# Kernel optimization log

Hardware: AMD Instinct MI355X
Metric: run time of the kernel (lower is better)

## Reference

```python
import jax, jax.numpy as jnp
import numpy as np

BLOCK_SIZE = 32
HEADS = 8
DIM_HEAD = 64
ROPE_THETA = 10000.0


def rmsnorm(x, w):
    eps = jnp.finfo(x.dtype).eps
    var = jnp.mean(jnp.square(x), axis=-1, keepdims=True)
    return x * jax.lax.rsqrt(var + eps) * w


def rope_cos_sin(seq_len, dim_head):
    # lucidrains rotary-embedding-torch default: interleaved pairs, theta=10000
    inv_freq = 1.0 / (ROPE_THETA ** (jnp.arange(0, dim_head, 2, dtype=jnp.float32) / dim_head))
    freqs = jnp.arange(seq_len, dtype=jnp.float32)[:, None] * inv_freq[None, :]  # [S, Dh/2]
    return jnp.cos(freqs), jnp.sin(freqs)


def apply_rope(t, cos, sin):
    # t: [B, H, S, Dh], cos/sin: [S, Dh/2]
    t1 = t[..., 0::2]
    t2 = t[..., 1::2]
    out = jnp.stack([t1 * cos - t2 * sin, t1 * sin + t2 * cos], axis=-1)
    return out.reshape(t.shape)


def split_heads(x, h):
    b, n, _ = x.shape
    return x.reshape(b, n, h, -1).transpose(0, 2, 1, 3)  # b h n d


def forward(tokens, attn_norm_w, qkv_w, out_w, mix_w, mix_b,
            ff_norm_w, ff_in_w, ff_in_b, ff_out_w, ff_out_b, final_norm_w):
    B, S, D = tokens.shape
    L = qkv_w.shape[0]
    H, Dh = HEADS, DIM_HEAD
    scale = Dh ** -0.5
    cos, sin = rope_cos_sin(S, Dh)

    # block-causal mask: q_idx // block >= kv_idx // block
    idx = jnp.arange(S)
    allowed = (idx[:, None] // BLOCK_SIZE) >= (idx[None, :] // BLOCK_SIZE)  # [S, S] bool
    neg = -jnp.finfo(tokens.dtype).max

    t = tokens
    first_v = None
    for l in range(L):
        # --- block causal attention ---
        x = rmsnorm(t, attn_norm_w[l])
        qkv = x @ qkv_w[l]  # [B, S, 3*H*Dh]
        q, k, v = jnp.split(qkv, 3, axis=-1)
        q, k, v = split_heads(q, H), split_heads(k, H), split_heads(v, H)  # b h s d
        orig_v = v
        if l > 0:
            mix = jax.nn.sigmoid(x @ mix_w[l] + mix_b[l])  # [B, S, H]
            mix = mix.transpose(0, 2, 1)[..., None]  # [B, H, S, 1]
            v = v + mix * (first_v - v)  # lerp
        q = apply_rope(q, cos, sin)
        k = apply_rope(k, cos, sin)
        sim = jnp.einsum('bhid,bhjd->bhij', q * scale, k)
        sim = jnp.where(allowed, sim, neg)
        attn = jax.nn.softmax(sim, axis=-1)
        o = jnp.einsum('bhij,bhjd->bhid', attn, v)
        o = o.transpose(0, 2, 1, 3).reshape(B, S, H * Dh)
        t = t + o @ out_w[l]
        if first_v is None:
            first_v = orig_v
        # --- SwiGLU feedforward ---
        y = rmsnorm(t, ff_norm_w[l])
        h = y @ ff_in_w[l] + ff_in_b[l]
        a, g = jnp.split(h, 2, axis=-1)
        y = (a * jax.nn.gelu(g, approximate=False)) @ ff_out_w[l] + ff_out_b[l]
        t = t + y

    return rmsnorm(t, final_norm_w)


def setup_inputs():
    key = jax.random.key(0)
    B, S, D, L = 2, 2048, 512, 4
    Di = HEADS * DIM_HEAD  # 512
    Dhid = int(D * 4.0 * 2 / 3)  # 1365
    ks = jax.random.split(key, 8)
    s = 0.02
    return {
        'tokens': jax.random.normal(ks[0], (B, S, D), jnp.float32),
        'attn_norm_w': jnp.ones((L, D), jnp.float32),
        'qkv_w': jax.random.normal(ks[1], (L, D, 3 * Di), jnp.float32) * s,
        'out_w': jax.random.normal(ks[2], (L, Di, D), jnp.float32) * s,
        'mix_w': jax.random.normal(ks[3], (L, D, HEADS), jnp.float32) * s,
        'mix_b': jnp.zeros((L, HEADS), jnp.float32),
        'ff_norm_w': jnp.ones((L, D), jnp.float32),
        'ff_in_w': jax.random.normal(ks[4], (L, D, 2 * Dhid), jnp.float32) * s,
        'ff_in_b': jnp.zeros((L, 2 * Dhid), jnp.float32),
        'ff_out_w': jax.random.normal(ks[5], (L, Dhid, D), jnp.float32) * s,
        'ff_out_b': jnp.zeros((L, D), jnp.float32),
        'final_norm_w': jnp.ones((D,), jnp.float32),
    }


def reference(tokens, attn_norm_w, qkv_w, out_w, mix_w, mix_b,
              ff_norm_w, ff_in_w, ff_in_b, ff_out_w, ff_out_b, final_norm_w):
    return forward(tokens, attn_norm_w, qkv_w, out_w, mix_w, mix_b,
                   ff_norm_w, ff_in_w, ff_in_b, ff_out_w, ff_out_b, final_norm_w)
```

## Files before the change

kernel.cpp:

```cpp
#include <hip/hip_runtime.h>
#include <hip/hip_bf16.h>
#include <math.h>

typedef __bf16 bf16;
typedef bf16 bf16x8 __attribute__((ext_vector_type(8)));
typedef float f32x4 __attribute__((ext_vector_type(4)));

#define LDS16(gp, lp) __builtin_amdgcn_global_load_lds( \
    (const __attribute__((address_space(1))) unsigned int*)(gp), \
    (__attribute__((address_space(3))) unsigned int*)(lp), 16, 0, 0)

__device__ __forceinline__ int cumoff2(int qtp) {
  if (qtp < 4)  return qtp;
  if (qtp < 8)  return 4 + 2 * (qtp - 4);
  if (qtp < 12) return 12 + 3 * (qtp - 8);
  return 24 + 4 * (qtp - 12);
}

__global__ void convert_w_kernel(const float* __restrict__ W, bf16* __restrict__ WT,
                                 int K, int N, int Kp, int Np,
                                 size_t wstride, size_t wtstride)
{
  __shared__ float tile[32][33];
  const float* Wl = W + blockIdx.z * wstride;
  bf16* WTl = WT + blockIdx.z * wtstride;
  int k0 = blockIdx.x * 32, n0 = blockIdx.y * 32;
  int tx = threadIdx.x, ty = threadIdx.y;
  for (int i = ty; i < 32; i += 8) {
    int k = k0 + i, n = n0 + tx;
    tile[i][tx] = (k < K && n < N) ? Wl[(size_t)k * N + n] : 0.f;
  }
  __syncthreads();
  for (int i = ty; i < 32; i += 8) {
    int n = n0 + i, k = k0 + tx;
    if (n < Np && k < Kp) WTl[(size_t)n * Kp + k] = (bf16)tile[tx][i];
  }
}

__global__ void convert_w_ffin_kernel(const float* __restrict__ W, bf16* __restrict__ WT)
{
  __shared__ float tile[32][33];
  const float* Wl = W + (size_t)blockIdx.z * 512 * 2730;
  bf16* WTl = WT + (size_t)blockIdx.z * 2816 * 512;
  int k0 = blockIdx.x * 32, n0 = blockIdx.y * 32;
  int tx = threadIdx.x, ty = threadIdx.y;
  for (int i = ty; i < 32; i += 8) {
    int k = k0 + i, n = n0 + tx;
    int pair = n >> 1;
    int col = (n & 1) ? 1365 + pair : pair;
    tile[i][tx] = (pair < 1365) ? Wl[(size_t)k * 2730 + col] : 0.f;
  }
  __syncthreads();
  for (int i = ty; i < 32; i += 8) {
    int n = n0 + i, k = k0 + tx;
    WTl[(size_t)n * 512 + k] = (bf16)tile[tx][i];
  }
}

__global__ __launch_bounds__(256)
void ibias_kernel(const float* __restrict__ ffib, float* __restrict__ ib)
{
  int idx = blockIdx.x * 256 + threadIdx.x;
  int l = idx / 2816, n = idx - l * 2816;
  int pair = n >> 1;
  int col = (n & 1) ? 1365 + pair : pair;
  ib[idx] = (pair < 1365) ? ffib[l * 2730 + col] : 0.f;
}

__global__ __launch_bounds__(256)
void rope_kernel(float* __restrict__ tab)
{
  int idx = blockIdx.x * 256 + threadIdx.x;
  int s = idx >> 5, j = idx & 31;
  float invf = (float)exp((double)(2 * j) * -0.14391156847064293);
  float ang = (float)s * invf;
  float sn, cs;
  sincosf(ang, &sn, &cs);
  tab[idx] = cs;
  tab[65536 + idx] = sn;
}

template<bool BF16OUT>
__global__ __launch_bounds__(256)
void rmsnorm_kernel(const float* __restrict__ in, const float* __restrict__ wgt,
                    void* __restrict__ outp)
{
  int row = blockIdx.x * 4 + (threadIdx.x >> 6);
  int lane = threadIdx.x & 63;
  const float* p = in + (size_t)row * 512;
  float4 v0 = *(const float4*)(p + lane * 4);
  float4 v1 = *(const float4*)(p + 256 + lane * 4);
  float ss = v0.x*v0.x + v0.y*v0.y + v0.z*v0.z + v0.w*v0.w
           + v1.x*v1.x + v1.y*v1.y + v1.z*v1.z + v1.w*v1.w;
  #pragma unroll
  for (int d = 1; d < 64; d <<= 1) ss += __shfl_xor(ss, d);
  float sc = rsqrtf(ss * (1.f / 512.f) + 1.1920929e-7f);
  float a0[4] = {v0.x, v0.y, v0.z, v0.w};
  float a1[4] = {v1.x, v1.y, v1.z, v1.w};
  #pragma unroll
  for (int i = 0; i < 4; ++i) {
    int c0 = lane * 4 + i, c1 = 256 + lane * 4 + i;
    float r0 = a0[i] * sc * wgt[c0];
    float r1 = a1[i] * sc * wgt[c1];
    if (BF16OUT) {
      ((bf16*)outp)[(size_t)row * 512 + c0] = (bf16)r0;
      ((bf16*)outp)[(size_t)row * 512 + c1] = (bf16)r1;
    } else {
      ((float*)outp)[(size_t)row * 512 + c0] = r0;
      ((float*)outp)[(size_t)row * 512 + c1] = r1;
    }
  }
}

__global__ __launch_bounds__(256, 4)
void qkvpost_kernel(const bf16* __restrict__ qkv, const float* __restrict__ mb,
                    const float* __restrict__ rope, bf16* __restrict__ firstv,
                    bf16* __restrict__ qb, bf16* __restrict__ kb,
                    bf16* __restrict__ vT, int layer)
{
  __shared__ float smv[64][65];
  const int st = blockIdx.x, bh = blockIdx.y;
  const int b = bh >> 3, h = bh & 7;
  const int tid = threadIdx.x;
  const int sl = tid >> 2, dg = tid & 3;
  const int s = st * 64 + sl;
  const size_t row = (size_t)b * 2048 + s;
  const bf16* base = qkv + row * 1664 + h * 64 + dg * 16;

  bf16x8 qv0 = *(const bf16x8*)(base);
  bf16x8 qv1 = *(const bf16x8*)(base + 8);
  bf16x8 kv0 = *(const bf16x8*)(base + 512);
  bf16x8 kv1 = *(const bf16x8*)(base + 520);
  bf16x8 vv0 = *(const bf16x8*)(base + 1024);
  bf16x8 vv1 = *(const bf16x8*)(base + 1032);

  float cs8[8], sn8[8];
  #pragma unroll
  for (int j = 0; j < 8; ++j) {
    cs8[j] = rope[s * 32 + dg * 8 + j];
    sn8[j] = rope[65536 + s * 32 + dg * 8 + j];
  }

  const size_t qoff = ((size_t)bh * 2048 + s) * 64 + dg * 16;
  bf16x8 oq0, oq1, ok0, ok1;
  #pragma unroll
  for (int p = 0; p < 4; ++p) {
    float q1 = (float)qv0[2 * p], q2 = (float)qv0[2 * p + 1];
    float k1 = (float)kv0[2 * p], k2 = (float)kv0[2 * p + 1];
    oq0[2 * p]     = (bf16)((q1 * cs8[p] - q2 * sn8[p]) * 0.125f);
    oq0[2 * p + 1] = (bf16)((q1 * sn8[p] + q2 * cs8[p]) * 0.125f);
    ok0[2 * p]     = (bf16)(k1 * cs8[p] - k2 * sn8[p]);
    ok0[2 * p + 1] = (bf16)(k1 * sn8[p] + k2 * cs8[p]);
    float q3 = (float)qv1[2 * p], q4v = (float)qv1[2 * p + 1];
    float k3 = (float)kv1[2 * p], k4 = (float)kv1[2 * p + 1];
    oq1[2 * p]     = (bf16)((q3 * cs8[p + 4] - q4v * sn8[p + 4]) * 0.125f);
    oq1[2 * p + 1] = (bf16)((q3 * sn8[p + 4] + q4v * cs8[p + 4]) * 0.125f);
    ok1[2 * p]     = (bf16)(k3 * cs8[p + 4] - k4 * sn8[p + 4]);
    ok1[2 * p + 1] = (bf16)(k3 * sn8[p + 4] + k4 * cs8[p + 4]);
  }
  *(bf16x8*)(qb + qoff)     = oq0;
  *(bf16x8*)(qb + qoff + 8) = oq1;
  *(bf16x8*)(kb + qoff)     = ok0;
  *(bf16x8*)(kb + qoff + 8) = ok1;

  float vout[16];
  #pragma unroll
  for (int i = 0; i < 8; ++i) { vout[i] = (float)vv0[i]; vout[8 + i] = (float)vv1[i]; }
  if (layer == 0) {
    *(bf16x8*)(firstv + qoff)     = vv0;
    *(bf16x8*)(firstv + qoff + 8) = vv1;
  } else {
    float logit = (float)qkv[row * 1664 + 1536 + h] + mb[h];
    float mx = 1.f / (1.f + __expf(-logit));
    bf16x8 fv0 = *(const bf16x8*)(firstv + qoff);
    bf16x8 fv1 = *(const bf16x8*)(firstv + qoff + 8);
    #pragma unroll
    for (int i = 0; i < 8; ++i) {
      vout[i]     += mx * ((float)fv0[i] - vout[i]);
      vout[8 + i] += mx * ((float)fv1[i] - vout[8 + i]);
    }
  }
  #pragma unroll
  for (int i = 0; i < 16; ++i)
    smv[sl][dg * 16 + i] = vout[i];

  __syncthreads();

  const int d = tid >> 2, q4 = tid & 3;
  bf16x8 o0, o1;
  #pragma unroll
  for (int i = 0; i < 8; ++i) {
    o0[i] = (bf16)smv[q4 * 16 + i][d];
    o1[i] = (bf16)smv[q4 * 16 + 8 + i][d];
  }
  bf16* vp = vT + ((size_t)bh * 64 + d) * 2048 + st * 64 + q4 * 16;
  *(bf16x8*)(vp)     = o0;
  *(bf16x8*)(vp + 8) = o1;
}

__global__ __launch_bounds__(256, 2)
void attn_kernel(const bf16* __restrict__ Q, const bf16* __restrict__ Kmat,
                 const bf16* __restrict__ VT, bf16* __restrict__ Opart,
                 float* __restrict__ lbuf)
{
  __shared__ __align__(16) bf16 smK[3][8 * 512];
  __shared__ __align__(16) bf16 smV[3][8 * 512];
  __shared__ __align__(16) bf16 smP[4][2][16 * 72];
  const int bid = blockIdx.x;
  const int bh = bid & 15;
  const int cidx = bid >> 4;
  int qtp, chunk;
  if (cidx < 4)       { qtp = cidx; chunk = 0; }
  else if (cidx < 12) { qtp = 4 + ((cidx - 4) >> 1);  chunk = (cidx - 4) & 1; }
  else if (cidx < 24) { int t = cidx - 12; qtp = 8 + t / 3; chunk = t - (qtp - 8) * 3; }
  else                { int t = cidx - 24; qtp = 12 + (t >> 2); chunk = t & 3; }
  const int jt0 = chunk * 8;
  const int njt = min(jt0 + 8, 2 * qtp + 2) - jt0;

  const int tid = threadIdx.x;
  const int w = tid >> 6, lane = tid & 63;
  const int c = lane & 15, quad = lane >> 4;
  const int jtmax_w = (qtp * 4 + w) >> 1;

  const size_t qrow0 = (size_t)bh * 2048 + qtp * 128 + w * 32;
  bf16x8 aQ[2][2];
  #pragma unroll
  for (int m = 0; m < 2; ++m) {
    aQ[m][0] = *(const bf16x8*)(Q + (qrow0 + m * 16 + c) * 64 + quad * 8);
    aQ[m][1] = *(const bf16x8*)(Q + (qrow0 + m * 16 + c) * 64 + 32 + quad * 8);
  }

  const bf16* Kg = Kmat + ((size_t)bh * 2048 + w * 16 + c) * 64 + quad * 8;
  const bf16* Vg = VT + ((size_t)bh * 64 + w * 16 + c) * 2048 + quad * 8;

  auto stage = [&](int tile, int buf) {
    const bf16* kp = Kg + (size_t)tile * 4096;
    const bf16* vp = Vg + tile * 64;
    bf16* kd = smK[buf] + w * 1024;
    bf16* vd = smV[buf] + w * 1024;
    LDS16(kp,      kd);
    LDS16(kp + 32, kd + 512);
    LDS16(vp,      vd);
    LDS16(vp + 32, vd + 512);
  };
  stage(jt0, 0);
  if (njt > 1) stage(jt0 + 1, 1);

  f32x4 o[2][4] = {};
  float lacc[2][4] = {};

  for (int j = 0; j < njt; ++j) {
    const int bufc = j % 3;
    const int jt = jt0 + j;
    if (j + 1 < njt) asm volatile("s_waitcnt vmcnt(4)\n\ts_barrier" ::: "memory");
    else             asm volatile("s_waitcnt vmcnt(0)\n\ts_barrier" ::: "memory");
    if (j + 2 < njt) stage(jt0 + j + 2, (j + 2) % 3);
    if (jt > jtmax_w) continue;

    f32x4 s[2][4];
    #pragma unroll
    for (int nt = 0; nt < 4; ++nt) {
      bf16x8 bK0 = *(const bf16x8*)(smK[bufc] + (nt * 2) * 512 + lane * 8);
      bf16x8 bK1 = *(const bf16x8*)(smK[bufc] + (nt * 2 + 1) * 512 + lane * 8);
      #pragma unroll
      for (int m = 0; m < 2; ++m) {
        f32x4 acc = {0.f, 0.f, 0.f, 0.f};
        acc = __builtin_amdgcn_mfma_f32_16x16x32_bf16(aQ[m][0], bK0, acc, 0, 0, 0);
        acc = __builtin_amdgcn_mfma_f32_16x16x32_bf16(aQ[m][1], bK1, acc, 0, 0, 0);
        s[m][nt] = acc;
      }
    }
    if (2 * jt + 1 > 4 * qtp + w) {
      #pragma unroll
      for (int m = 0; m < 2; ++m)
        #pragma unroll
        for (int r = 0; r < 4; ++r) { s[m][2][r] = -3.0e38f; s[m][3][r] = -3.0e38f; }
    }

    #pragma unroll
    for (int m = 0; m < 2; ++m) {
      #pragma unroll
      for (int r = 0; r < 4; ++r) {
        float p0 = __expf(s[m][0][r]);
        float p1 = __expf(s[m][1][r]);
        float p2 = __expf(s[m][2][r]);
        float p3 = __expf(s[m][3][r]);
        lacc[m][r] += (p0 + p1) + (p2 + p3);
        bf16* pp = smP[w][m] + (quad * 4 + r) * 72 + c;
        pp[0]  = (bf16)p0;
        pp[16] = (bf16)p1;
        pp[32] = (bf16)p2;
        pp[48] = (bf16)p3;
      }
    }
    asm volatile("s_waitcnt lgkmcnt(0)" ::: "memory");

    #pragma unroll
    for (int ks2 = 0; ks2 < 2; ++ks2) {
      #pragma unroll
      for (int m = 0; m < 2; ++m) {
        bf16x8 aP = *(const bf16x8*)(smP[w][m] + c * 72 + ks2 * 32 + quad * 8);
        #pragma unroll
        for (int nt = 0; nt < 4; ++nt) {
          bf16x8 bV = *(const bf16x8*)(smV[bufc] + (nt * 2 + ks2) * 512 + lane * 8);
          o[m][nt] = __builtin_amdgcn_mfma_f32_16x16x32_bf16(aP, bV, o[m][nt], 0, 0, 0);
        }
      }
    }
  }

  #pragma unroll
  for (int m = 0; m < 2; ++m)
    #pragma unroll
    for (int r = 0; r < 4; ++r) {
      float v = lacc[m][r];
      #pragma unroll
      for (int d = 1; d < 16; d <<= 1) v += __shfl_xor(v, d);
      lacc[m][r] = v;
    }

  const int slot = bh * 40 + cumoff2(qtp) + chunk;
  bf16* Op = Opart + (size_t)slot * 8192;
  #pragma unroll
  for (int m = 0; m < 2; ++m) {
    #pragma unroll
    for (int r = 0; r < 4; ++r) {
      int prow = w * 32 + m * 16 + quad * 4 + r;
      #pragma unroll
      for (int nt = 0; nt < 4; ++nt)
        Op[prow * 64 + nt * 16 + c] = (bf16)o[m][nt][r];
      if (c == 0) lbuf[slot * 128 + prow] = lacc[m][r];
    }
  }
}

__global__ __launch_bounds__(256)
void attn_combine_kernel(const bf16* __restrict__ Opart, const float* __restrict__ lbuf,
                         bf16* __restrict__ Omat)
{
  const int qt = blockIdx.x, bh = blockIdx.y;
  const int qtp = qt >> 1;
  const int nch = (2 * qtp + 9) >> 3;
  const int base = bh * 40 + cumoff2(qtp);
  const int tid = threadIdx.x;
  const int row = tid >> 2, cg = tid & 3;
  const int prow = (qt & 1) * 64 + row;

  float L = 0.f;
  float acc[16] = {};
  #pragma unroll
  for (int ch = 0; ch < 4; ++ch) {
    if (ch < nch) {
      L += lbuf[(base + ch) * 128 + prow];
      const bf16* p = Opart + (size_t)(base + ch) * 8192 + prow * 64 + cg * 16;
      bf16x8 u0 = *(const bf16x8*)(p);
      bf16x8 u1 = *(const bf16x8*)(p + 8);
      #pragma unroll
      for (int i = 0; i < 8; ++i) { acc[i] += (float)u0[i]; acc[8 + i] += (float)u1[i]; }
    }
  }
  float inv = 1.f / L;

  const int b = bh >> 3, h = bh & 7;
  bf16* op = Omat + ((size_t)b * 2048 + qt * 64 + row) * 512 + h * 64 + cg * 16;
  #pragma unroll
  for (int i = 0; i < 16; ++i)
    op[i] = (bf16)(acc[i] * inv);
}

template<int MODE>
__global__ __launch_bounds__(256, 2)
void gemm_kernel(const bf16* __restrict__ A, const bf16* __restrict__ WT,
                 const float* __restrict__ bias, int n_bias,
                 const float* __restrict__ Tin, void* __restrict__ outp,
                 int K, int N)
{
  __shared__ __align__(16) bf16 smA[8 * 512];
  __shared__ __align__(16) bf16 smB[8 * 512];
  const int tid = threadIdx.x;
  const int w = tid >> 6, lane = tid & 63;
  const int c = lane & 15, quad = lane >> 4;
  const int wy = w >> 1, wx = w & 1;
  const int bm = blockIdx.y * 128, bn = blockIdx.x * 128;

  f32x4 acc[4][4] = {};

  const bf16* Ag0 = A  + (size_t)(bm + (w * 2)     * 16 + c) * K + quad * 8;
  const bf16* Ag1 = A  + (size_t)(bm + (w * 2 + 1) * 16 + c) * K + quad * 8;
  const bf16* Bg0 = WT + (size_t)(bn + (w * 2)     * 16 + c) * K + quad * 8;
  const bf16* Bg1 = WT + (size_t)(bn + (w * 2 + 1) * 16 + c) * K + quad * 8;
  bf16* la0 = smA + (w * 2) * 512;
  bf16* la1 = smA + (w * 2 + 1) * 512;
  bf16* lb0 = smB + (w * 2) * 512;
  bf16* lb1 = smB + (w * 2 + 1) * 512;

  const int NK = K >> 5;
  for (int kk = 0; kk < NK; ++kk) {
    const int ko = kk * 32;
    LDS16(Ag0 + ko, la0);
    LDS16(Ag1 + ko, la1);
    LDS16(Bg0 + ko, lb0);
    LDS16(Bg1 + ko, lb1);
    __syncthreads();
    bf16x8 af[4], bfr[4];
    #pragma unroll
    for (int mt = 0; mt < 4; ++mt)
      af[mt] = *(const bf16x8*)(smA + (wy * 4 + mt) * 512 + lane * 8);
    #pragma unroll
    for (int nt = 0; nt < 4; ++nt)
      bfr[nt] = *(const bf16x8*)(smB + (wx * 4 + nt) * 512 + lane * 8);
    #pragma unroll
    for (int mt = 0; mt < 4; ++mt)
      #pragma unroll
      for (int nt = 0; nt < 4; ++nt)
        acc[mt][nt] = __builtin_amdgcn_mfma_f32_16x16x32_bf16(af[mt], bfr[nt], acc[mt][nt], 0, 0, 0);
    __syncthreads();
  }

  const int r0 = bm + wy * 64;
  const int c0 = bn + wx * 64;
  #pragma unroll
  for (int mt = 0; mt < 4; ++mt) {
    #pragma unroll
    for (int nt = 0; nt < 4; ++nt) {
      #pragma unroll
      for (int r = 0; r < 4; ++r) {
        size_t row = (size_t)(r0 + mt * 16 + quad * 4 + r);
        int col = c0 + nt * 16 + c;
        float v = acc[mt][nt][r];
        if (MODE == 3) {
          v += bias[col];
          float g = __shfl_xor(v, 1);
          if ((c & 1) == 0) {
            float outv = v * 0.5f * g * (1.f + erff(g * 0.70710678118654752f));
            ((bf16*)outp)[row * (size_t)(N >> 1) + (col >> 1)] = (bf16)outv;
          }
        } else {
          float bv = (bias != nullptr && col < n_bias) ? bias[col] : 0.f;
          if (MODE == 2) {
            ((float*)outp)[row * N + col] = Tin[row * N + col] + v + bv;
          } else {
            ((bf16*)outp)[row * N + col] = (bf16)(v + bv);
          }
        }
      }
    }
  }
}

template<int MODE>
__global__ __launch_bounds__(256, 4)
void gemm64_kernel(const bf16* __restrict__ A, const bf16* __restrict__ WT,
                   const float* __restrict__ bias, int n_bias,
                   const float* __restrict__ Tin, void* __restrict__ outp,
                   int K, int N)
{
  __shared__ __align__(16) bf16 smA[4 * 512];
  __shared__ __align__(16) bf16 smB[4 * 512];
  const int tid = threadIdx.x;
  const int w = tid >> 6, lane = tid & 63;
  const int c = lane & 15, quad = lane >> 4;
  const int wy = w >> 1, wx = w & 1;
  const int bm = blockIdx.y * 64, bn = blockIdx.x * 64;

  f32x4 acc[2][2] = {};

  const bf16* Ag = A  + (size_t)(bm + w * 16 + c) * K + quad * 8;
  const bf16* Bg = WT + (size_t)(bn + w * 16 + c) * K + quad * 8;
  bf16* la = smA + w * 512;
  bf16* lb = smB + w * 512;

  const int NK = K >> 5;
  for (int kk = 0; kk < NK; ++kk) {
    const int ko = kk * 32;
    LDS16(Ag + ko, la);
    LDS16(Bg + ko, lb);
    __syncthreads();
    bf16x8 af[2], bfr[2];
    #pragma unroll
    for (int mt = 0; mt < 2; ++mt)
      af[mt] = *(const bf16x8*)(smA + (wy * 2 + mt) * 512 + lane * 8);
    #pragma unroll
    for (int nt = 0; nt < 2; ++nt)
      bfr[nt] = *(const bf16x8*)(smB + (wx * 2 + nt) * 512 + lane * 8);
    #pragma unroll
    for (int mt = 0; mt < 2; ++mt)
      #pragma unroll
      for (int nt = 0; nt < 2; ++nt)
        acc[mt][nt] = __builtin_amdgcn_mfma_f32_16x16x32_bf16(af[mt], bfr[nt], acc[mt][nt], 0, 0, 0);
    __syncthreads();
  }

  const int r0 = bm + wy * 32;
  const int c0 = bn + wx * 32;
  #pragma unroll
  for (int mt = 0; mt < 2; ++mt) {
    #pragma unroll
    for (int nt = 0; nt < 2; ++nt) {
      #pragma unroll
      for (int r = 0; r < 4; ++r) {
        size_t row = (size_t)(r0 + mt * 16 + quad * 4 + r);
        int col = c0 + nt * 16 + c;
        float v = acc[mt][nt][r];
        float bv = (bias != nullptr && col < n_bias) ? bias[col] : 0.f;
        if (MODE == 2) {
          ((float*)outp)[row * N + col] = Tin[row * N + col] + v + bv;
        } else {
          ((bf16*)outp)[row * N + col] = (bf16)(v + bv);
        }
      }
    }
  }
}

extern "C" void kernel_launch(void* const* d_in, const int* in_sizes, int n_in,
                              void* d_out, int out_size, void* d_ws, size_t ws_size,
                              hipStream_t stream)
{
  const float* tokens  = (const float*)d_in[0];
  const float* anw     = (const float*)d_in[1];
  const float* qkvw    = (const float*)d_in[2];
  const float* outw    = (const float*)d_in[3];
  const float* mixw    = (const float*)d_in[4];
  const float* mixbias = (const float*)d_in[5];
  const float* fnw     = (const float*)d_in[6];
  const float* ffiw    = (const float*)d_in[7];
  const float* ffib    = (const float*)d_in[8];
  const float* ffow    = (const float*)d_in[9];
  const float* ffob    = (const float*)d_in[10];
  const float* finw    = (const float*)d_in[11];
  float* outp = (float*)d_out;

  char* ws = (char*)d_ws;
  size_t off = 0;
  auto alloc = [&](size_t bytes) -> char* {
    char* p = ws + off;
    off += (bytes + 255) & ~(size_t)255;
    return p;
  };
  bf16* wtq    = (bf16*)alloc((size_t)4 * 1664 * 512 * 2);
  bf16* wto    = (bf16*)alloc((size_t)4 * 512 * 512 * 2);
  bf16* wtfi   = (bf16*)alloc((size_t)4 * 2816 * 512 * 2);
  bf16* wtfo   = (bf16*)alloc((size_t)4 * 512 * 1408 * 2);
  float* ibias = (float*)alloc((size_t)4 * 2816 * 4);
  float* tbuf  = (float*)alloc((size_t)4096 * 512 * 4);
  bf16* xb     = (bf16*)alloc((size_t)4096 * 512 * 2);
  bf16* yb     = (bf16*)alloc((size_t)4096 * 512 * 2);
  char* qkvraw = alloc((size_t)4096 * 1664 * 2);
  bf16* fv     = (bf16*)alloc((size_t)16 * 2048 * 64 * 2);
  bf16* qb     = (bf16*)alloc((size_t)16 * 2048 * 64 * 2);
  bf16* kbuf   = (bf16*)alloc((size_t)16 * 2048 * 64 * 2);
  bf16* vT     = (bf16*)alloc((size_t)16 * 2048 * 64 * 2);
  bf16* ob     = (bf16*)alloc((size_t)4096 * 512 * 2);
  bf16* actb   = (bf16*)alloc((size_t)4096 * 1408 * 2);
  float* rope  = (float*)alloc((size_t)2 * 65536 * 4);
  float* lbuf  = (float*)alloc((size_t)640 * 128 * 4);
  bf16* qkvbf  = (bf16*)qkvraw;
  bf16* Opart  = (bf16*)qkvraw;

  dim3 tcv(32, 8);
  convert_w_kernel<<<dim3(16, 48, 4), tcv, 0, stream>>>(
      qkvw, wtq, 512, 1536, 512, 1536, (size_t)512 * 1536, (size_t)1664 * 512);
  convert_w_kernel<<<dim3(16, 4, 4), tcv, 0, stream>>>(
      mixw, wtq + (size_t)1536 * 512, 512, 8, 512, 128, (size_t)512 * 8, (size_t)1664 * 512);
  convert_w_kernel<<<dim3(16, 16, 4), tcv, 0, stream>>>(
      outw, wto, 512, 512, 512, 512, (size_t)512 * 512, (size_t)512 * 512);
  convert_w_ffin_kernel<<<dim3(16, 88, 4), tcv, 0, stream>>>(ffiw, wtfi);
  convert_w_kernel<<<dim3(44, 16, 4), tcv, 0, stream>>>(
      ffow, wtfo, 1365, 512, 1408, 512, (size_t)1365 * 512, (size_t)1408 * 512);
  ibias_kernel<<<44, 256, 0, stream>>>(ffib, ibias);
  rope_kernel<<<256, 256, 0, stream>>>(rope);
  hipMemcpyAsync(tbuf, tokens, (size_t)4096 * 512 * 4, hipMemcpyDeviceToDevice, stream);

  for (int l = 0; l < 4; ++l) {
    rmsnorm_kernel<true><<<1024, 256, 0, stream>>>(tbuf, anw + l * 512, xb);
    gemm_kernel<0><<<dim3(13, 32), 256, 0, stream>>>(
        xb, wtq + (size_t)l * 1664 * 512, nullptr, 0, nullptr, qkvbf, 512, 1664);
    qkvpost_kernel<<<dim3(32, 16), 256, 0, stream>>>(qkvbf, mixbias + l * 8, rope, fv, qb, kbuf, vT, l);
    attn_kernel<<<640, 256, 0, stream>>>(qb, kbuf, vT, Opart, lbuf);
    attn_combine_kernel<<<dim3(32, 16), 256, 0, stream>>>(Opart, lbuf, ob);
    gemm64_kernel<2><<<dim3(8, 64), 256, 0, stream>>>(
        ob, wto + (size_t)l * 512 * 512, nullptr, 0, tbuf, tbuf, 512, 512);
    rmsnorm_kernel<true><<<1024, 256, 0, stream>>>(tbuf, fnw + l * 512, yb);
    gemm_kernel<3><<<dim3(22, 32), 256, 0, stream>>>(
        yb, wtfi + (size_t)l * 2816 * 512, ibias + (size_t)l * 2816, 2816, nullptr, actb, 512, 2816);
    gemm64_kernel<2><<<dim3(8, 64), 256, 0, stream>>>(
        actb, wtfo + (size_t)l * 512 * 1408, ffob + (size_t)l * 512, 512, tbuf, tbuf, 1408, 512);
  }
  rmsnorm_kernel<false><<<1024, 256, 0, stream>>>(tbuf, finw, outp);
}
```

Baseline: 770.8 us.

## Fold RMSNorm into GEMM epilogues and double-buffer attention K/V

```diff
diff --git a/kernel.cpp b/kernel.cpp
--- a/kernel.cpp
+++ b/kernel.cpp
@@ -18,6 +18,7 @@
 }
 
 __global__ void convert_w_kernel(const float* __restrict__ W, bf16* __restrict__ WT,
+                                 const float* __restrict__ ks,
                                  int K, int N, int Kp, int Np,
                                  size_t wstride, size_t wtstride)
 {
@@ -28,7 +29,9 @@
   int tx = threadIdx.x, ty = threadIdx.y;
   for (int i = ty; i < 32; i += 8) {
     int k = k0 + i, n = n0 + tx;
-    tile[i][tx] = (k < K && n < N) ? Wl[(size_t)k * N + n] : 0.f;
+    float v = (k < K && n < N) ? Wl[(size_t)k * N + n] : 0.f;
+    if (ks && k < K) v *= ks[blockIdx.z * K + k];
+    tile[i][tx] = v;
   }
   __syncthreads();
   for (int i = ty; i < 32; i += 8) {
@@ -37,7 +40,8 @@
   }
 }
 
-__global__ void convert_w_ffin_kernel(const float* __restrict__ W, bf16* __restrict__ WT)
+__global__ void convert_w_ffin_kernel(const float* __restrict__ W, bf16* __restrict__ WT,
+                                      const float* __restrict__ fnw)
 {
   __shared__ float tile[32][33];
   const float* Wl = W + (size_t)blockIdx.z * 512 * 2730;
@@ -48,7 +52,8 @@
     int k = k0 + i, n = n0 + tx;
     int pair = n >> 1;
     int col = (n & 1) ? 1365 + pair : pair;
-    tile[i][tx] = (pair < 1365) ? Wl[(size_t)k * 2730 + col] : 0.f;
+    float v = (pair < 1365) ? Wl[(size_t)k * 2730 + col] : 0.f;
+    tile[i][tx] = v * fnw[blockIdx.z * 512 + k];
   }
   __syncthreads();
   for (int i = ty; i < 32; i += 8) {
@@ -80,10 +85,32 @@
   tab[65536 + idx] = sn;
 }
 
-template<bool BF16OUT>
+__global__ __launch_bounds__(256)
+void init_kernel(const float* __restrict__ tok, bf16* __restrict__ xb,
+                 float* __restrict__ sumsq)
+{
+  int row = blockIdx.x * 4 + (threadIdx.x >> 6);
+  int lane = threadIdx.x & 63;
+  const float* p = tok + (size_t)row * 512;
+  float4 v0 = *(const float4*)(p + lane * 4);
+  float4 v1 = *(const float4*)(p + 256 + lane * 4);
+  float ss = v0.x*v0.x + v0.y*v0.y + v0.z*v0.z + v0.w*v0.w
+           + v1.x*v1.x + v1.y*v1.y + v1.z*v1.z + v1.w*v1.w;
+  #pragma unroll
+  for (int d = 1; d < 64; d <<= 1) ss += __shfl_xor(ss, d);
+  float a0[4] = {v0.x, v0.y, v0.z, v0.w};
+  float a1[4] = {v1.x, v1.y, v1.z, v1.w};
+  #pragma unroll
+  for (int i = 0; i < 4; ++i) {
+    xb[(size_t)row * 512 + lane * 4 + i]       = (bf16)a0[i];
+    xb[(size_t)row * 512 + 256 + lane * 4 + i] = (bf16)a1[i];
+  }
+  if (lane == 0) sumsq[row] = ss;
+}
+
 __global__ __launch_bounds__(256)
 void rmsnorm_kernel(const float* __restrict__ in, const float* __restrict__ wgt,
-                    void* __restrict__ outp)
+                    float* __restrict__ outp)
 {
   int row = blockIdx.x * 4 + (threadIdx.x >> 6);
   int lane = threadIdx.x & 63;
@@ -100,15 +127,8 @@
   #pragma unroll
   for (int i = 0; i < 4; ++i) {
     int c0 = lane * 4 + i, c1 = 256 + lane * 4 + i;
-    float r0 = a0[i] * sc * wgt[c0];
-    float r1 = a1[i] * sc * wgt[c1];
-    if (BF16OUT) {
-      ((bf16*)outp)[(size_t)row * 512 + c0] = (bf16)r0;
-      ((bf16*)outp)[(size_t)row * 512 + c1] = (bf16)r1;
-    } else {
-      ((float*)outp)[(size_t)row * 512 + c0] = r0;
-      ((float*)outp)[(size_t)row * 512 + c1] = r1;
-    }
+    outp[(size_t)row * 512 + c0] = a0[i] * sc * wgt[c0];
+    outp[(size_t)row * 512 + c1] = a1[i] * sc * wgt[c1];
   }
 }
 
@@ -198,13 +218,13 @@
   *(bf16x8*)(vp + 8) = o1;
 }
 
-__global__ __launch_bounds__(256, 2)
+__global__ __launch_bounds__(256, 3)
 void attn_kernel(const bf16* __restrict__ Q, const bf16* __restrict__ Kmat,
                  const bf16* __restrict__ VT, bf16* __restrict__ Opart,
                  float* __restrict__ lbuf)
 {
-  __shared__ __align__(16) bf16 smK[3][8 * 512];
-  __shared__ __align__(16) bf16 smV[3][8 * 512];
+  __shared__ __align__(16) bf16 smK[2][8 * 512];
+  __shared__ __align__(16) bf16 smV[2][8 * 512];
   __shared__ __align__(16) bf16 smP[4][2][16 * 72];
   const int bid = blockIdx.x;
   const int bh = bid & 15;
@@ -233,35 +253,39 @@
   const bf16* Kg = Kmat + ((size_t)bh * 2048 + w * 16 + c) * 64 + quad * 8;
   const bf16* Vg = VT + ((size_t)bh * 64 + w * 16 + c) * 2048 + quad * 8;
 
-  auto stage = [&](int tile, int buf) {
-    const bf16* kp = Kg + (size_t)tile * 4096;
-    const bf16* vp = Vg + tile * 64;
-    bf16* kd = smK[buf] + w * 1024;
-    bf16* vd = smV[buf] + w * 1024;
-    LDS16(kp,      kd);
-    LDS16(kp + 32, kd + 512);
-    LDS16(vp,      vd);
-    LDS16(vp + 32, vd + 512);
-  };
-  stage(jt0, 0);
-  if (njt > 1) stage(jt0 + 1, 1);
+  {
+    const bf16* kp = Kg + (size_t)jt0 * 4096;
+    const bf16* vp = Vg + jt0 * 64;
+    LDS16(kp,      smK[0] + w * 1024);
+    LDS16(kp + 32, smK[0] + w * 1024 + 512);
+    LDS16(vp,      smV[0] + w * 1024);
+    LDS16(vp + 32, smV[0] + w * 1024 + 512);
+  }
 
   f32x4 o[2][4] = {};
   float lacc[2][4] = {};
 
   for (int j = 0; j < njt; ++j) {
-    const int bufc = j % 3;
+    const int b = j & 1;
     const int jt = jt0 + j;
-    if (j + 1 < njt) asm volatile("s_waitcnt vmcnt(4)\n\ts_barrier" ::: "memory");
-    else             asm volatile("s_waitcnt vmcnt(0)\n\ts_barrier" ::: "memory");
-    if (j + 2 < njt) stage(jt0 + j + 2, (j + 2) % 3);
+    __syncthreads();
+    if (j + 1 < njt) {
+      const bf16* kp = Kg + (size_t)(jt + 1) * 4096;
+      const bf16* vp = Vg + (jt + 1) * 64;
+      bf16* kd = smK[1 - b] + w * 1024;
+      bf16* vd = smV[1 - b] + w * 1024;
+      LDS16(kp,      kd);
+      LDS16(kp + 32, kd + 512);
+      LDS16(vp,      vd);
+      LDS16(vp + 32, vd + 512);
+    }
     if (jt > jtmax_w) continue;
 
     f32x4 s[2][4];
     #pragma unroll
     for (int nt = 0; nt < 4; ++nt) {
-      bf16x8 bK0 = *(const bf16x8*)(smK[bufc] + (nt * 2) * 512 + lane * 8);
-      bf16x8 bK1 = *(const bf16x8*)(smK[bufc] + (nt * 2 + 1) * 512 + lane * 8);
+      bf16x8 bK0 = *(const bf16x8*)(smK[b] + (nt * 2) * 512 + lane * 8);
+      bf16x8 bK1 = *(const bf16x8*)(smK[b] + (nt * 2 + 1) * 512 + lane * 8);
       #pragma unroll
       for (int m = 0; m < 2; ++m) {
         f32x4 acc = {0.f, 0.f, 0.f, 0.f};
@@ -302,7 +326,7 @@
         bf16x8 aP = *(const bf16x8*)(smP[w][m] + c * 72 + ks2 * 32 + quad * 8);
         #pragma unroll
         for (int nt = 0; nt < 4; ++nt) {
-          bf16x8 bV = *(const bf16x8*)(smV[bufc] + (nt * 2 + ks2) * 512 + lane * 8);
+          bf16x8 bV = *(const bf16x8*)(smV[b] + (nt * 2 + ks2) * 512 + lane * 8);
           o[m][nt] = __builtin_amdgcn_mfma_f32_16x16x32_bf16(aP, bV, o[m][nt], 0, 0, 0);
         }
       }
@@ -371,13 +395,16 @@
 template<int MODE>
 __global__ __launch_bounds__(256, 2)
 void gemm_kernel(const bf16* __restrict__ A, const bf16* __restrict__ WT,
-                 const float* __restrict__ bias, int n_bias,
-                 const float* __restrict__ Tin, void* __restrict__ outp,
+                 const float* __restrict__ bias, const float* __restrict__ sumsq,
+                 float* __restrict__ zbuf, void* __restrict__ outp,
                  int K, int N)
 {
   __shared__ __align__(16) bf16 smA[8 * 512];
   __shared__ __align__(16) bf16 smB[8 * 512];
   const int tid = threadIdx.x;
+  if (blockIdx.x == 0 && blockIdx.y == 0) {
+    for (int i = tid; i < 4096; i += 256) zbuf[i] = 0.f;
+  }
   const int w = tid >> 6, lane = tid & 63;
   const int c = lane & 15, quad = lane >> 4;
   const int wy = w >> 1, wx = w & 1;
@@ -422,12 +449,13 @@
   #pragma unroll
   for (int mt = 0; mt < 4; ++mt) {
     #pragma unroll
-    for (int nt = 0; nt < 4; ++nt) {
-      #pragma unroll
-      for (int r = 0; r < 4; ++r) {
-        size_t row = (size_t)(r0 + mt * 16 + quad * 4 + r);
+    for (int r = 0; r < 4; ++r) {
+      size_t row = (size_t)(r0 + mt * 16 + quad * 4 + r);
+      float sc = rsqrtf(sumsq[row] * (1.f / 512.f) + 1.1920929e-7f);
+      #pragma unroll
+      for (int nt = 0; nt < 4; ++nt) {
         int col = c0 + nt * 16 + c;
-        float v = acc[mt][nt][r];
+        float v = acc[mt][nt][r] * sc;
         if (MODE == 3) {
           v += bias[col];
           float g = __shfl_xor(v, 1);
@@ -436,24 +464,18 @@
             ((bf16*)outp)[row * (size_t)(N >> 1) + (col >> 1)] = (bf16)outv;
           }
         } else {
-          float bv = (bias != nullptr && col < n_bias) ? bias[col] : 0.f;
-          if (MODE == 2) {
-            ((float*)outp)[row * N + col] = Tin[row * N + col] + v + bv;
-          } else {
-            ((bf16*)outp)[row * N + col] = (bf16)(v + bv);
-          }
+          ((bf16*)outp)[row * N + col] = (bf16)v;
         }
       }
     }
   }
 }
 
-template<int MODE>
 __global__ __launch_bounds__(256, 4)
 void gemm64_kernel(const bf16* __restrict__ A, const bf16* __restrict__ WT,
-                   const float* __restrict__ bias, int n_bias,
-                   const float* __restrict__ Tin, void* __restrict__ outp,
-                   int K, int N)
+                   const float* __restrict__ bias, const float* __restrict__ Tin,
+                   float* __restrict__ outf, bf16* __restrict__ bcopy,
+                   float* __restrict__ sumsq, int K)
 {
   __shared__ __align__(16) bf16 smA[4 * 512];
   __shared__ __align__(16) bf16 smB[4 * 512];
@@ -493,6 +515,7 @@
 
   const int r0 = bm + wy * 32;
   const int c0 = bn + wx * 32;
+  float ssq[2][4] = {};
   #pragma unroll
   for (int mt = 0; mt < 2; ++mt) {
     #pragma unroll
@@ -501,16 +524,24 @@
       for (int r = 0; r < 4; ++r) {
         size_t row = (size_t)(r0 + mt * 16 + quad * 4 + r);
         int col = c0 + nt * 16 + c;
-        float v = acc[mt][nt][r];
-        float bv = (bias != nullptr && col < n_bias) ? bias[col] : 0.f;
-        if (MODE == 2) {
-          ((float*)outp)[row * N + col] = Tin[row * N + col] + v + bv;
-        } else {
-          ((bf16*)outp)[row * N + col] = (bf16)(v + bv);
-        }
+        float bv = (bias != nullptr) ? bias[col] : 0.f;
+        float v = Tin[row * 512 + col] + acc[mt][nt][r] + bv;
+        outf[row * 512 + col] = v;
+        bcopy[row * 512 + col] = (bf16)v;
+        ssq[mt][r] += v * v;
       }
     }
   }
+  #pragma unroll
+  for (int mt = 0; mt < 2; ++mt)
+    #pragma unroll
+    for (int r = 0; r < 4; ++r) {
+      float v = ssq[mt][r];
+      #pragma unroll
+      for (int d = 1; d < 16; d <<= 1) v += __shfl_xor(v, d);
+      if (c == 0)
+        atomicAdd(&sumsq[r0 + mt * 16 + quad * 4 + r], v);
+    }
 }
 
 extern "C" void kernel_launch(void* const* d_in, const int* in_sizes, int n_in,
@@ -555,37 +586,40 @@
   bf16* actb   = (bf16*)alloc((size_t)4096 * 1408 * 2);
   float* rope  = (float*)alloc((size_t)2 * 65536 * 4);
   float* lbuf  = (float*)alloc((size_t)640 * 128 * 4);
+  float* ssqa  = (float*)alloc((size_t)4096 * 4);
+  float* ssqb  = (float*)alloc((size_t)4096 * 4);
   bf16* qkvbf  = (bf16*)qkvraw;
   bf16* Opart  = (bf16*)qkvraw;
 
   dim3 tcv(32, 8);
   convert_w_kernel<<<dim3(16, 48, 4), tcv, 0, stream>>>(
-      qkvw, wtq, 512, 1536, 512, 1536, (size_t)512 * 1536, (size_t)1664 * 512);
+      qkvw, wtq, anw, 512, 1536, 512, 1536, (size_t)512 * 1536, (size_t)1664 * 512);
   convert_w_kernel<<<dim3(16, 4, 4), tcv, 0, stream>>>(
-      mixw, wtq + (size_t)1536 * 512, 512, 8, 512, 128, (size_t)512 * 8, (size_t)1664 * 512);
+      mixw, wtq + (size_t)1536 * 512, anw, 512, 8, 512, 128, (size_t)512 * 8, (size_t)1664 * 512);
   convert_w_kernel<<<dim3(16, 16, 4), tcv, 0, stream>>>(
-      outw, wto, 512, 512, 512, 512, (size_t)512 * 512, (size_t)512 * 512);
-  convert_w_ffin_kernel<<<dim3(16, 88, 4), tcv, 0, stream>>>(ffiw, wtfi);
+      outw, wto, nullptr, 512, 512, 512, 512, (size_t)512 * 512, (size_t)512 * 512);
+  convert_w_ffin_kernel<<<dim3(16, 88, 4), tcv, 0, stream>>>(ffiw, wtfi, fnw);
   convert_w_kernel<<<dim3(44, 16, 4), tcv, 0, stream>>>(
-      ffow, wtfo, 1365, 512, 1408, 512, (size_t)1365 * 512, (size_t)1408 * 512);
+      ffow, wtfo, nullptr, 1365, 512, 1408, 512, (size_t)1365 * 512, (size_t)1408 * 512);
   ibias_kernel<<<44, 256, 0, stream>>>(ffib, ibias);
   rope_kernel<<<256, 256, 0, stream>>>(rope);
-  hipMemcpyAsync(tbuf, tokens, (size_t)4096 * 512 * 4, hipMemcpyDeviceToDevice, stream);
+  init_kernel<<<1024, 256, 0, stream>>>(tokens, xb, ssqa);
 
   for (int l = 0; l < 4; ++l) {
-    rmsnorm_kernel<true><<<1024, 256, 0, stream>>>(tbuf, anw + l * 512, xb);
     gemm_kernel<0><<<dim3(13, 32), 256, 0, stream>>>(
-        xb, wtq + (size_t)l * 1664 * 512, nullptr, 0, nullptr, qkvbf, 512, 1664);
-    qkvpost_kernel<<<dim3(32, 16), 256, 0, stream>>>(qkvbf, mixbias + l * 8, rope, fv, qb, kbuf, vT, l);
+        xb, wtq + (size_t)l * 1664 * 512, nullptr, ssqa, ssqb, qkvbf, 512, 1664);
+    qkvpost_kernel<<<dim3(32, 16), 256, 0, stream>>>(
+        qkvbf, mixbias + l * 8, rope, fv, qb, kbuf, vT, l);
     attn_kernel<<<640, 256, 0, stream>>>(qb, kbuf, vT, Opart, lbuf);
     attn_combine_kernel<<<dim3(32, 16), 256, 0, stream>>>(Opart, lbuf, ob);
-    gemm64_kernel<2><<<dim3(8, 64), 256, 0, stream>>>(
-        ob, wto + (size_t)l * 512 * 512, nullptr, 0, tbuf, tbuf, 512, 512);
-    rmsnorm_kernel<true><<<1024, 256, 0, stream>>>(tbuf, fnw + l * 512, yb);
+    gemm64_kernel<<<dim3(8, 64), 256, 0, stream>>>(
+        ob, wto + (size_t)l * 512 * 512, nullptr, (l == 0) ? tokens : tbuf,
+        tbuf, yb, ssqb, 512);
     gemm_kernel<3><<<dim3(22, 32), 256, 0, stream>>>(
-        yb, wtfi + (size_t)l * 2816 * 512, ibias + (size_t)l * 2816, 2816, nullptr, actb, 512, 2816);
-    gemm64_kernel<2><<<dim3(8, 64), 256, 0, stream>>>(
-        actb, wtfo + (size_t)l * 512 * 1408, ffob + (size_t)l * 512, 512, tbuf, tbuf, 1408, 512);
-  }
-  rmsnorm_kernel<false><<<1024, 256, 0, stream>>>(tbuf, finw, outp);
-}
+        yb, wtfi + (size_t)l * 2816 * 512, ibias + (size_t)l * 2816, ssqb, ssqa, actb, 512, 2816);
+    gemm64_kernel<<<dim3(8, 64), 256, 0, stream>>>(
+        actb, wtfo + (size_t)l * 512 * 1408, ffob + (size_t)l * 512, tbuf,
+        tbuf, xb, ssqa, 1408);
+  }
+  rmsnorm_kernel<<<1024, 256, 0, stream>>>(tbuf, finw, outp);
+}
```

Measured after the change: 717.1 us. 7.0% less time.
